# Performance work log

Hardware: AMD Instinct MI355X
Metric: run time of the kernel (lower is better)

## Reference

```python
import jax, jax.numpy as jnp
import numpy as np

jax.config.update("jax_enable_x64", True)  # original casts to double for covpool/SVD

BN_EPS = 1e-5


def setup_inputs() -> dict:
    key = jax.random.key(0)
    k1, k2 = jax.random.split(key)
    x = jax.random.normal(k1, (64, 2048, 14, 14), dtype=jnp.float32)
    conv_w = jax.random.normal(k2, (256, 2048), dtype=jnp.float32) * 0.02  # 1x1 conv kernel
    bn_gamma = jnp.ones((256,), dtype=jnp.float32)
    bn_beta = jnp.zeros((256,), dtype=jnp.float32)
    return {"x": x, "conv_w": conv_w, "bn_gamma": bn_gamma, "bn_beta": bn_beta}


def reference(x, conv_w, bn_gamma, bn_beta):
    # --- dimension reduction block: 1x1 conv (no bias) + BN (train mode) + ReLU ---
    y = jnp.einsum('oc,bchw->bohw', conv_w, x)  # [B,256,14,14]
    mean = y.mean(axis=(0, 2, 3), keepdims=True)
    var = y.var(axis=(0, 2, 3), keepdims=True)
    y = (y - mean) * jax.lax.rsqrt(var + BN_EPS)
    y = y * bn_gamma[None, :, None, None] + bn_beta[None, :, None, None]
    y = jnp.maximum(y, 0.0)

    # --- Covpool: x @ (I/M - 11^T/M^2) @ x^T, in float64 as original ---
    B, d, h, w = y.shape
    M = h * w
    z = y.reshape(B, d, M).astype(jnp.float64)
    zc = z - z.mean(axis=2, keepdims=True)          # centering == multiplying by I_hat
    cov = jnp.einsum('bim,bjm->bij', zc, zc) / M    # [B,d,d], symmetric PSD

    # --- Eigen decomposition (SVD of symmetric PSD == eigh), clamp tiny eigvals ---
    s, V = jnp.linalg.eigh(cov)                     # s: [B,d], V: [B,d,d]
    eps = jnp.finfo(jnp.float64).eps
    s = jnp.maximum(s, eps)

    # --- Power: matrix square root Q = V sqrt(S) V^T ---
    Q = jnp.einsum('bij,bj,bkj->bik', V, jnp.sqrt(s), V)  # [B,d,d]

    # --- upper-triangular (incl. diag) vectorization, row-major like torch triu ---
    iu = jnp.triu_indices(d)
    q_triv = Q[:, iu[0], iu[1]]                     # [B, d*(d+1)/2]
    return q_triv.astype(jnp.float32)
```

## Files before the change

kernel.cpp:

```cpp
#include <hip/hip_runtime.h>
#include <hip/hip_bf16.h>

static constexpr int B   = 64;
static constexpr int CIN = 2048;
static constexpr int O   = 256;
static constexpr int HW  = 196;
static constexpr int D   = 256;
static constexpr int TRI = 32896;
static constexpr int NQ_COUPLED = 5;
static constexpr size_t NELEM = (size_t)B * D * D;
static constexpr size_t YN    = (size_t)B * O * HW;

typedef unsigned short u16;
typedef unsigned short u16x4 __attribute__((ext_vector_type(4)));
typedef unsigned short u16x8 __attribute__((ext_vector_type(8)));
typedef __bf16         bf16x8 __attribute__((ext_vector_type(8)));
typedef float          f32x4 __attribute__((ext_vector_type(4)));

static __device__ __forceinline__ u16 f2bf(float x) {
    unsigned int u = __float_as_uint(x);
    u += 0x7FFFu + ((u >> 16) & 1u);
    return (u16)(u >> 16);
}
static __device__ __forceinline__ float bf2f(u16 h) {
    return __uint_as_float(((unsigned int)h) << 16);
}
static __device__ __forceinline__ f32x4 mm_bf16(u16x8 a, u16x8 b, f32x4 c) {
    return __builtin_amdgcn_mfma_f32_16x16x32_bf16(
        __builtin_bit_cast(bf16x8, a), __builtin_bit_cast(bf16x8, b), c, 0, 0, 0);
}

__global__ __launch_bounds__(256) void k_wsplit(const float* __restrict__ W,
                                                u16* __restrict__ Wh,
                                                u16* __restrict__ Wl) {
    const size_t i = (size_t)blockIdx.x * 256 + threadIdx.x;
    const float v = W[i];
    const u16 h = f2bf(v);
    Wh[i] = h;
    Wl[i] = f2bf(v - bf2f(h));
}

__global__ __launch_bounds__(256, 3) void k_conv(const float* __restrict__ x,
                                                 const u16* __restrict__ Wh,
                                                 const u16* __restrict__ Wl,
                                                 float* __restrict__ psum) {
    const int l   = blockIdx.x;
    const int xcd = l & 7, u = l >> 3;
    const int q   = xcd * 98 + u;
    const int ks  = q & 3;
    const int t2  = q >> 2;
    const int ot  = t2 & 1, gt = t2 >> 1;
    const int o0  = ot * 128;
    const int cbase = ks * 512;
    float* yp = psum + (size_t)ks * YN;

    const int tid = threadIdx.x;

    __shared__ u16 sW[2][128][40], sX[2][128][40];

    const int colX  = tid & 127;
    const int chalf = (tid >> 7) * 16;
    const int gX = gt * 128 + colX;
    const int bX = gX / 196;
    const int mX = gX - bX * 196;
    const size_t xbase = (size_t)bX * (CIN * HW) + mX;

    const int rW = tid >> 1, kq = (tid & 1) * 16;
    const u16* gWh = Wh + (size_t)(o0 + rW) * CIN + cbase + kq;
    const u16* gWl = Wl + (size_t)(o0 + rW) * CIN + cbase + kq;

    const int lane = tid & 63, w = tid >> 6;
    const int wr = w >> 1, wc = w & 1;
    const int lr = lane & 15, lg = lane >> 4, ko = lg << 3;

    f32x4 acc[4][4] = {};

    u16x8 pWh[2], pWl[2];
    float pX[16];
    u16x4 cXh[4], cXl[4];

    auto loadW = [&](int kb) {
        #pragma unroll
        for (int qq = 0; qq < 2; ++qq) {
            pWh[qq] = *(const u16x8*)&gWh[kb + qq * 8];
            pWl[qq] = *(const u16x8*)&gWl[kb + qq * 8];
        }
    };
    auto loadX = [&](int kb) {
        #pragma unroll
        for (int i = 0; i < 16; ++i)
            pX[i] = x[xbase + (size_t)(cbase + kb + chalf + i) * HW];
    };
    auto convX = [&]() {
        #pragma unroll
        for (int i = 0; i < 16; i += 4) {
            u16x4 vh, vl;
            #pragma unroll
            for (int j = 0; j < 4; ++j) {
                const float v = pX[i + j];
                const u16 h = f2bf(v);
                vh[j] = h;
                vl[j] = f2bf(v - bf2f(h));
            }
            cXh[i >> 2] = vh;
            cXl[i >> 2] = vl;
        }
    };
    auto storeWX = [&]() {
        #pragma unroll
        for (int qq = 0; qq < 2; ++qq) {
            *(u16x8*)&sW[0][rW][kq + qq * 8] = pWh[qq];
            *(u16x8*)&sW[1][rW][kq + qq * 8] = pWl[qq];
        }
        #pragma unroll
        for (int qq = 0; qq < 4; ++qq) {
            *(u16x4*)&sX[0][colX][chalf + qq * 4] = cXh[qq];
            *(u16x4*)&sX[1][colX][chalf + qq * 4] = cXl[qq];
        }
    };
    auto compute = [&]() {
        u16x8 fah[4], fal[4], fbh[4], fbl[4];
        #pragma unroll
        for (int f = 0; f < 4; ++f) {
            fah[f] = *(const u16x8*)&sW[0][wr * 64 + f * 16 + lr][ko];
            fal[f] = *(const u16x8*)&sW[1][wr * 64 + f * 16 + lr][ko];
            fbh[f] = *(const u16x8*)&sX[0][wc * 64 + f * 16 + lr][ko];
            fbl[f] = *(const u16x8*)&sX[1][wc * 64 + f * 16 + lr][ko];
        }
        #pragma unroll
        for (int fi = 0; fi < 4; ++fi)
            #pragma unroll
            for (int fj = 0; fj < 4; ++fj) {
                acc[fi][fj] = mm_bf16(fah[fi], fbh[fj], acc[fi][fj]);
                acc[fi][fj] = mm_bf16(fah[fi], fbl[fj], acc[fi][fj]);
                acc[fi][fj] = mm_bf16(fal[fi], fbh[fj], acc[fi][fj]);
            }
    };

    loadW(0); loadX(0); convX();
    for (int st = 0; st < 16; ++st) {
        __syncthreads();
        storeWX();
        __syncthreads();
        if (st < 15) { loadW((st + 1) * 32); loadX((st + 1) * 32); }
        compute();
        if (st < 15) convX();
    }

    #pragma unroll
    for (int fj = 0; fj < 4; ++fj) {
        const int gcol = gt * 128 + wc * 64 + fj * 16 + lr;
        const int bb = gcol / 196;
        const int mm = gcol - bb * 196;
        const size_t ybase = (size_t)bb * (O * HW) + mm;
        #pragma unroll
        for (int fi = 0; fi < 4; ++fi)
            #pragma unroll
            for (int r = 0; r < 4; ++r) {
                const int orow = o0 + wr * 64 + fi * 16 + (lg << 2) + r;
                yp[ybase + (size_t)orow * HW] = acc[fi][fj][r];
            }
    }
}

__global__ __launch_bounds__(256) void k_redy(const float* __restrict__ ps,
                                              float* __restrict__ y) {
    const size_t i = ((size_t)blockIdx.x * 256 + threadIdx.x) * 4;
    if (i >= YN) return;
    float4 a = *(const float4*)&ps[i];
    const float4 b = *(const float4*)&ps[YN + i];
    const float4 c = *(const float4*)&ps[2 * YN + i];
    const float4 d = *(const float4*)&ps[3 * YN + i];
    a.x += b.x + c.x + d.x; a.y += b.y + c.y + d.y;
    a.z += b.z + c.z + d.z; a.w += b.w + c.w + d.w;
    *(float4*)&y[i] = a;
}

__global__ __launch_bounds__(256) void k_bnstats(const float* __restrict__ y,
                                                 const float* __restrict__ gamma,
                                                 const float* __restrict__ beta,
                                                 float* __restrict__ scl,
                                                 float* __restrict__ shf) {
    const int o = blockIdx.x;
    const int tid = threadIdx.x;
    float s = 0.f, s2 = 0.f;
    if (tid < HW) {
        for (int b = 0; b < B; ++b) {
            const float v = y[((size_t)b * O + o) * HW + tid];
            s += v; s2 += v * v;
        }
    }
    #pragma unroll
    for (int msk = 32; msk; msk >>= 1) {
        s  += __shfl_xor(s,  msk);
        s2 += __shfl_xor(s2, msk);
    }
    __shared__ float rs[4], rs2[4];
    if ((tid & 63) == 0) { rs[tid >> 6] = s; rs2[tid >> 6] = s2; }
    __syncthreads();
    if (tid == 0) {
        const float N = (float)(B * HW);
        const float ts  = rs[0] + rs[1] + rs[2] + rs[3];
        const float ts2 = rs2[0] + rs2[1] + rs2[2] + rs2[3];
        const float mean = ts / N;
        const float var  = ts2 / N - mean * mean;
        const float sc = gamma[o] * rsqrtf(var + 1e-5f);
        scl[o] = sc;
        shf[o] = beta[o] - mean * sc;
    }
}

__global__ __launch_bounds__(64) void k_center(float* __restrict__ z,
                                               const float* __restrict__ scl,
                                               const float* __restrict__ shf) {
    const int row = blockIdx.x;
    const int o = row & 255;
    const int lane = threadIdx.x;
    const float sc = scl[o], sh = shf[o];
    float* zr = &z[(size_t)row * HW];
    float vals[4];
    float s = 0.f;
    #pragma unroll
    for (int q = 0; q < 4; ++q) {
        const int m = q * 64 + lane;
        float v = 0.f;
        if (m < HW) v = fmaxf(fmaf(zr[m], sc, sh), 0.f);
        vals[q] = v; s += v;
    }
    #pragma unroll
    for (int msk = 32; msk; msk >>= 1) s += __shfl_xor(s, msk);
    const float mean = s / (float)HW;
    #pragma unroll
    for (int q = 0; q < 4; ++q) {
        const int m = q * 64 + lane;
        if (m < HW) zr[m] = vals[q] - mean;
    }
}

__global__ __launch_bounds__(256) void k_cov(const float* __restrict__ z,
                                             float* __restrict__ covf) {
    const int b = blockIdx.y;
    const int jt = blockIdx.x & 3, it = blockIdx.x >> 2;
    const int i0 = it * 64, j0 = jt * 64;
    const int tid = threadIdx.x;
    const int tn = tid & 15, tmq = tid >> 4;

    __shared__ float sA[28][68], sB[28][68];
    double acc[4][4] = {};
    const float* zb = &z[(size_t)b * D * HW];

    for (int k0 = 0; k0 < HW; k0 += 28) {
        #pragma unroll
        for (int q = 0; q < 7; ++q) {
            const int idx = tid + q * 256;
            const int r = idx / 28, kk = idx % 28;
            sA[kk][r] = zb[(size_t)(i0 + r) * HW + k0 + kk];
            sB[kk][r] = zb[(size_t)(j0 + r) * HW + k0 + kk];
        }
        __syncthreads();
        #pragma unroll
        for (int kk = 0; kk < 28; ++kk) {
            const float4 av = *reinterpret_cast<const float4*>(&sA[kk][tmq << 2]);
            const float4 bv = *reinterpret_cast<const float4*>(&sB[kk][tn << 2]);
            const double aa[4] = {av.x, av.y, av.z, av.w};
            const double bb[4] = {bv.x, bv.y, bv.z, bv.w};
            #pragma unroll
            for (int i = 0; i < 4; ++i)
                #pragma unroll
                for (int j = 0; j < 4; ++j)
                    acc[i][j] = fma(aa[i], bb[j], acc[i][j]);
        }
        __syncthreads();
    }
    const double inv = 1.0 / (double)HW;
    #pragma unroll
    for (int i = 0; i < 4; ++i)
        #pragma unroll
        for (int j = 0; j < 4; ++j)
            covf[(size_t)b * D * D + (size_t)(i0 + (tmq << 2) + i) * D
                 + j0 + (tn << 2) + j] = (float)(acc[i][j] * inv);
}

__global__ __launch_bounds__(256) void k_lmax(const float* __restrict__ covf,
                                              double* __restrict__ cn) {
    const int b = blockIdx.x;
    const int tid = threadIdx.x;
    const float* A = &covf[(size_t)b * 65536];
    __shared__ float vs[256];
    __shared__ float red[4];
    vs[tid] = 1.f;
    __syncthreads();
    float lam = 1.f;
    for (int it = 0; it < 6; ++it) {
        float u0 = 0.f, u1 = 0.f, u2 = 0.f, u3 = 0.f;
        #pragma unroll 8
        for (int k = 0; k < D; k += 4) {
            u0 = fmaf(A[(size_t)(k + 0) * D + tid], vs[k + 0], u0);
            u1 = fmaf(A[(size_t)(k + 1) * D + tid], vs[k + 1], u1);
            u2 = fmaf(A[(size_t)(k + 2) * D + tid], vs[k + 2], u2);
            u3 = fmaf(A[(size_t)(k + 3) * D + tid], vs[k + 3], u3);
        }
        const float uu = (u0 + u1) + (u2 + u3);
        float sq = uu * uu;
        #pragma unroll
        for (int msk = 32; msk; msk >>= 1) sq += __shfl_xor(sq, msk);
        __syncthreads();
        if ((tid & 63) == 0) red[tid >> 6] = sq;
        __syncthreads();
        const float nrm = sqrtf(red[0] + red[1] + red[2] + red[3]) + 1e-30f;
        lam = nrm;
        vs[tid] = uu / nrm;
        __syncthreads();
    }
    if (tid == 0) cn[b] = (lam > 1e-30f) ? 1.25 * (double)lam : 1.0;
}

__global__ __launch_bounds__(256) void k_init(const float* __restrict__ covf,
                                              const double* __restrict__ cn,
                                              u16* __restrict__ Yh,
                                              u16* __restrict__ Yl) {
    const size_t e = (size_t)blockIdx.x * 256 + threadIdx.x;
    const int b = (int)(e >> 16);
    const int ij = (int)(e & 65535);
    const float diag = ((ij >> 8) == (ij & 255)) ? 1e-7f : 0.f;
    const float f = covf[e] / (float)cn[b] + diag;
    const u16 h = f2bf(f);
    Yh[e] = h;
    Yl[e] = f2bf(f - bf2f(h));
}

template <int MODE, int FUSED>
__global__ __launch_bounds__(256, 2) void k_mgemm(
        const u16* __restrict__ A0h, const u16* __restrict__ A0l,
        const u16* __restrict__ B0h, const u16* __restrict__ B0l,
        u16* __restrict__ C0h, u16* __restrict__ C0l,
        const u16* __restrict__ A1h, const u16* __restrict__ A1l,
        const u16* __restrict__ B1h, const u16* __restrict__ B1l,
        u16* __restrict__ C1h, u16* __restrict__ C1l,
        const double* __restrict__ cn, float* __restrict__ outp) {
    const int orig = blockIdx.x;
    const int xcd  = orig & 7;
    const int s    = orig >> 3;
    int batch, task, opz;
    if (FUSED) {
        const int bl  = s / 12;
        const int rem = s - bl * 12;
        opz  = rem >= 6;
        task = rem - opz * 6;
        batch = xcd * 8 + bl;
    } else {
        opz = 0;
        const int bl = s / 6;
        task = s - bl * 6;
        batch = xcd * 8 + bl;
    }

    const u16 *Ah, *Al, *Bh, *Bl;
    u16 *Ch, *Cl;
    if (opz == 0) { Ah = A0h; Al = A0l; Bh = B0h; Bl = B0l; Ch = C0h; Cl = C0l; }
    else          { Ah = A1h; Al = A1l; Bh = B1h; Bl = B1l; Ch = C1h; Cl = C1l; }

    const int it = task >> 2;
    const int jt = (task < 4) ? task : task - 2;
    const int i0 = it * 128, j0 = jt * 64;
    const size_t boff = (size_t)batch * 65536;
    Ah += boff; Al += boff; Bh += boff; Bl += boff; Ch += boff; Cl += boff;

    const int tid = threadIdx.x;
    __shared__ u16 sA[2][128][72];
    __shared__ u16 sB[2][64][72];

    const int rA = tid >> 1, khA = (tid & 1) * 32;
    const u16* gAh = Ah + (size_t)(i0 + rA) * 256 + khA;
    const u16* gAl = Al + (size_t)(i0 + rA) * 256 + khA;
    const int rB = tid >> 2, khB = (tid & 3) * 16;
    const u16* gBh = Bh + (size_t)(j0 + rB) * 256 + khB;
    const u16* gBl = Bl + (size_t)(j0 + rB) * 256 + khB;

    const int lane = tid & 63, w = tid >> 6;
    const int wr = w >> 1, wc = w & 1;
    const int lr = lane & 15, lg = lane >> 4, ko = lg << 3;

    f32x4 acc[4][2] = {};

    u16x8 pAh[4], pAl[4], pBh[2], pBl[2];
    auto g_load = [&](int kb) {
        #pragma unroll
        for (int qq = 0; qq < 4; ++qq) {
            pAh[qq] = *(const u16x8*)&gAh[kb + qq * 8];
            pAl[qq] = *(const u16x8*)&gAl[kb + qq * 8];
        }
        #pragma unroll
        for (int qq = 0; qq < 2; ++qq) {
            pBh[qq] = *(const u16x8*)&gBh[kb + qq * 8];
            pBl[qq] = *(const u16x8*)&gBl[kb + qq * 8];
        }
    };
    auto s_store = [&]() {
        #pragma unroll
        for (int qq = 0; qq < 4; ++qq) {
            *(u16x8*)&sA[0][rA][khA + qq * 8] = pAh[qq];
            *(u16x8*)&sA[1][rA][khA + qq * 8] = pAl[qq];
        }
        #pragma unroll
        for (int qq = 0; qq < 2; ++qq) {
            *(u16x8*)&sB[0][rB][khB + qq * 8] = pBh[qq];
            *(u16x8*)&sB[1][rB][khB + qq * 8] = pBl[qq];
        }
    };
    auto compute = [&]() {
        #pragma unroll
        for (int kr = 0; kr < 2; ++kr) {
            const int kk = kr * 32 + ko;
            u16x8 fah[4], fal[4], fbh[2], fbl[2];
            #pragma unroll
            for (int f = 0; f < 4; ++f) {
                fah[f] = *(const u16x8*)&sA[0][wr * 64 + f * 16 + lr][kk];
                fal[f] = *(const u16x8*)&sA[1][wr * 64 + f * 16 + lr][kk];
            }
            #pragma unroll
            for (int f = 0; f < 2; ++f) {
                fbh[f] = *(const u16x8*)&sB[0][wc * 32 + f * 16 + lr][kk];
                fbl[f] = *(const u16x8*)&sB[1][wc * 32 + f * 16 + lr][kk];
            }
            #pragma unroll
            for (int fi = 0; fi < 4; ++fi)
                #pragma unroll
                for (int fj = 0; fj < 2; ++fj) {
                    acc[fi][fj] = mm_bf16(fah[fi], fbh[fj], acc[fi][fj]);
                    acc[fi][fj] = mm_bf16(fah[fi], fbl[fj], acc[fi][fj]);
                    acc[fi][fj] = mm_bf16(fal[fi], fbh[fj], acc[fi][fj]);
                }
        }
    };

    g_load(0);
    for (int st = 0; st < 4; ++st) {
        __syncthreads();
        s_store();
        __syncthreads();
        if (st < 3) g_load((st + 1) * 64);
        compute();
    }

    const int orow = wr * 64 + (lg << 2);
    const int ocol = wc * 32 + lr;

    if (MODE == 3) {
        const double sc = sqrt(cn[batch]);
        #pragma unroll
        for (int fi = 0; fi < 4; ++fi)
            #pragma unroll
            for (int r = 0; r < 4; ++r) {
                const int gi = i0 + orow + fi * 16 + r;
                const size_t rowoff = (size_t)gi * D - ((size_t)gi * (gi - 1)) / 2;
                #pragma unroll
                for (int fj = 0; fj < 2; ++fj) {
                    const int gj = j0 + ocol + fj * 16;
                    if (gj >= gi)
                        outp[(size_t)batch * TRI + rowoff + (gj - gi)] =
                            (float)(sc * (double)acc[fi][fj][r]);
                }
            }
        return;
    }

    u16 hv[4][4][2], lv[4][4][2];
    #pragma unroll
    for (int fi = 0; fi < 4; ++fi)
        #pragma unroll
        for (int r = 0; r < 4; ++r) {
            const int gi = i0 + orow + fi * 16 + r;
            #pragma unroll
            for (int fj = 0; fj < 2; ++fj) {
                const int gj = j0 + ocol + fj * 16;
                float v = acc[fi][fj][r];
                if (MODE == 1) {
                    const size_t xo = (size_t)gi * 256 + gj;
                    const float xv = bf2f(Ah[xo]) + bf2f(Al[xo]);
                    v = (((gi == gj) ? 15.0f : 0.0f) - 10.0f * xv + 3.0f * v) * 0.125f;
                }
                const u16 h = f2bf(v);
                const u16 lo = f2bf(v - bf2f(h));
                const size_t co = (size_t)gi * 256 + gj;
                Ch[co] = h;
                Cl[co] = lo;
                hv[fi][r][fj] = h;
                lv[fi][r][fj] = lo;
            }
        }

    if (task == 2 || task == 3) {
        __syncthreads();
        u16 (*tH)[136] = reinterpret_cast<u16(*)[136]>(&sA[0][0][0]);
        u16 (*tL)[136] = reinterpret_cast<u16(*)[136]>(&sB[0][0][0]);
        #pragma unroll
        for (int fi = 0; fi < 4; ++fi)
            #pragma unroll
            for (int r = 0; r < 4; ++r) {
                const int li = orow + fi * 16 + r;
                #pragma unroll
                for (int fj = 0; fj < 2; ++fj) {
                    const int lj = ocol + fj * 16;
                    tH[lj][li] = hv[fi][r][fj];
                    tL[lj][li] = lv[fi][r][fj];
                }
            }
        __syncthreads();
        const int r2 = tid >> 2, c2 = (tid & 3) << 5;
        const size_t mo = (size_t)(j0 + r2) * 256 + i0 + c2;
        #pragma unroll
        for (int qq = 0; qq < 4; ++qq) {
            *(u16x8*)&Ch[mo + qq * 8] = *(const u16x8*)&tH[r2][c2 + qq * 8];
            *(u16x8*)&Cl[mo + qq * 8] = *(const u16x8*)&tL[r2][c2 + qq * 8];
        }
    }
}

extern "C" void kernel_launch(void* const* d_in, const int* in_sizes, int n_in,
                              void* d_out, int out_size, void* d_ws, size_t ws_size,
                              hipStream_t stream) {
    const float* x     = (const float*)d_in[0];
    const float* W     = (const float*)d_in[1];
    const float* gamma = (const float*)d_in[2];
    const float* beta  = (const float*)d_in[3];
    float* out = (float*)d_out;

    char* ws = (char*)d_ws;
    size_t off = 0;
    auto alloc = [&](size_t bytes) -> void* {
        void* p = ws + off;
        off += (bytes + 255) & ~(size_t)255;
        return p;
    };
    float*  y    = (float*)alloc(YN * sizeof(float));
    float*  covf = (float*)alloc(NELEM * sizeof(float));
    float*  scl  = (float*)alloc(O * sizeof(float));
    float*  shf  = (float*)alloc(O * sizeof(float));
    double* cn   = (double*)alloc(B * sizeof(double));
    u16*    Wh   = (u16*)alloc((size_t)O * CIN * sizeof(u16));
    u16*    Wl   = (u16*)alloc((size_t)O * CIN * sizeof(u16));
    u16* pl = (u16*)alloc(12 * NELEM * sizeof(u16));
    if (off > ws_size) return;
    u16 *YAh = pl,             *YAl = pl + NELEM;
    u16 *YBh = pl + 2 * NELEM, *YBl = pl + 3 * NELEM;
    u16 *MAh = pl + 4 * NELEM, *MAl = pl + 5 * NELEM;
    u16 *MBh = pl + 6 * NELEM, *MBl = pl + 7 * NELEM;
    u16 *Rh  = pl + 8 * NELEM, *Rl  = pl + 9 * NELEM;
    u16 *Uh  = pl + 10 * NELEM,*Ul  = pl + 11 * NELEM;
    float* psum = (float*)pl;

    k_wsplit <<<(O * CIN) / 256, 256, 0, stream>>>(W, Wh, Wl);
    k_conv   <<<784, 256, 0, stream>>>(x, Wh, Wl, psum);
    k_redy   <<<3136, 256, 0, stream>>>(psum, y);
    k_bnstats<<<O, 256, 0, stream>>>(y, gamma, beta, scl, shf);
    k_center <<<B * O, 64, 0, stream>>>(y, scl, shf);
    k_cov    <<<dim3(16, B), 256, 0, stream>>>(y, covf);
    k_lmax   <<<B, 256, 0, stream>>>(covf, cn);
    k_init   <<<B * 256, 256, 0, stream>>>(covf, cn, YAh, YAl);

    k_mgemm<1, 0><<<384, 256, 0, stream>>>(YAh, YAl, YAh, YAl, Rh, Rl,
                                           YAh, YAl, YAh, YAl, Rh, Rl, cn, out);
    k_mgemm<2, 0><<<384, 256, 0, stream>>>(YAh, YAl, Rh, Rl, YBh, YBl,
                                           YAh, YAl, Rh, Rl, YBh, YBl, cn, out);
    k_mgemm<2, 0><<<384, 256, 0, stream>>>(Rh, Rl, YBh, YBl, MBh, MBl,
                                           Rh, Rl, YBh, YBl, MBh, MBl, cn, out);

    u16 *Ych = YBh, *Ycl = YBl, *Yah = YAh, *Yal = YAl;
    u16 *Mch = MBh, *Mcl = MBl, *Mah = MAh, *Mal = MAl;
    for (int itq = 0; itq < NQ_COUPLED; ++itq) {
        k_mgemm<1, 0><<<384, 256, 0, stream>>>(Mch, Mcl, Mch, Mcl, Rh, Rl,
                                               Mch, Mcl, Mch, Mcl, Rh, Rl, cn, out);
        k_mgemm<2, 1><<<768, 256, 0, stream>>>(Ych, Ycl, Rh, Rl, Yah, Yal,
                                               Mch, Mcl, Rh, Rl, Uh, Ul, cn, out);
        k_mgemm<2, 0><<<384, 256, 0, stream>>>(Rh, Rl, Uh, Ul, Mah, Mal,
                                               Rh, Rl, Uh, Ul, Mah, Mal, cn, out);
        u16* t;
        t = Ych; Ych = Yah; Yah = t;  t = Ycl; Ycl = Yal; Yal = t;
        t = Mch; Mch = Mah; Mah = t;  t = Mcl; Mcl = Mal; Mal = t;
    }
    k_mgemm<1, 0><<<384, 256, 0, stream>>>(Mch, Mcl, Mch, Mcl, Rh, Rl,
                                           Mch, Mcl, Mch, Mcl, Rh, Rl, cn, out);
    k_mgemm<3, 0><<<384, 256, 0, stream>>>(Ych, Ycl, Rh, Rl, Uh, Ul,
                                           Ych, Ycl, Rh, Rl, Uh, Ul, cn, out);
}
```

Before: 508.3 us.

## Fuse split-K reduction into BN stats, vectorize init, prefetch MODE1 operand

The split-K partial-sum reduction kernel is removed and folded into the BN statistics kernel, which now sums the four partials with float4 loads, writes y, and accumulates the mean and variance sums in the same pass. The init kernel handles four elements per thread with vector loads and stores. The MODE 1 GEMM loads its X operand before the main loop instead of in the epilogue, so those loads can overlap the compute. The trade-offs are that BN stats now runs only 256 blocks over the full partial buffer, and the prefetched values add registers to the GEMM.

```diff
diff --git a/kernel.cpp b/kernel.cpp
--- a/kernel.cpp
+++ b/kernel.cpp
@@ -163,20 +163,8 @@
     }
 }
 
-__global__ __launch_bounds__(256) void k_redy(const float* __restrict__ ps,
-                                              float* __restrict__ y) {
-    const size_t i = ((size_t)blockIdx.x * 256 + threadIdx.x) * 4;
-    if (i >= YN) return;
-    float4 a = *(const float4*)&ps[i];
-    const float4 b = *(const float4*)&ps[YN + i];
-    const float4 c = *(const float4*)&ps[2 * YN + i];
-    const float4 d = *(const float4*)&ps[3 * YN + i];
-    a.x += b.x + c.x + d.x; a.y += b.y + c.y + d.y;
-    a.z += b.z + c.z + d.z; a.w += b.w + c.w + d.w;
-    *(float4*)&y[i] = a;
-}
-
-__global__ __launch_bounds__(256) void k_bnstats(const float* __restrict__ y,
+__global__ __launch_bounds__(256) void k_bnstats(const float* __restrict__ ps,
+                                                 float* __restrict__ y,
                                                  const float* __restrict__ gamma,
                                                  const float* __restrict__ beta,
                                                  float* __restrict__ scl,
@@ -184,11 +172,18 @@
     const int o = blockIdx.x;
     const int tid = threadIdx.x;
     float s = 0.f, s2 = 0.f;
-    if (tid < HW) {
-        for (int b = 0; b < B; ++b) {
-            const float v = y[((size_t)b * O + o) * HW + tid];
-            s += v; s2 += v * v;
-        }
+    for (int t = tid; t < 64 * 49; t += 256) {
+        const int b = t / 49, c = t - b * 49;
+        const size_t idx = ((size_t)b * O + o) * HW + c * 4;
+        float4 a = *(const float4*)&ps[idx];
+        const float4 p1 = *(const float4*)&ps[YN + idx];
+        const float4 p2 = *(const float4*)&ps[2 * YN + idx];
+        const float4 p3 = *(const float4*)&ps[3 * YN + idx];
+        a.x += p1.x + p2.x + p3.x; a.y += p1.y + p2.y + p3.y;
+        a.z += p1.z + p2.z + p3.z; a.w += p1.w + p2.w + p3.w;
+        *(float4*)&y[idx] = a;
+        s  += (a.x + a.y) + (a.z + a.w);
+        s2 += (a.x * a.x + a.y * a.y) + (a.z * a.z + a.w * a.w);
     }
     #pragma unroll
     for (int msk = 32; msk; msk >>= 1) {
@@ -319,14 +314,24 @@
                                               const double* __restrict__ cn,
                                               u16* __restrict__ Yh,
                                               u16* __restrict__ Yl) {
-    const size_t e = (size_t)blockIdx.x * 256 + threadIdx.x;
-    const int b = (int)(e >> 16);
-    const int ij = (int)(e & 65535);
-    const float diag = ((ij >> 8) == (ij & 255)) ? 1e-7f : 0.f;
-    const float f = covf[e] / (float)cn[b] + diag;
-    const u16 h = f2bf(f);
-    Yh[e] = h;
-    Yl[e] = f2bf(f - bf2f(h));
+    const size_t e4 = ((size_t)blockIdx.x * 256 + threadIdx.x) * 4;
+    const int b = (int)(e4 >> 16);
+    const int ij = (int)(e4 & 65535);
+    const int i = ij >> 8, j0_ = ij & 255;
+    const float4 cv = *(const float4*)&covf[e4];
+    const float inv = 1.f / (float)cn[b];
+    float f[4] = {cv.x * inv, cv.y * inv, cv.z * inv, cv.w * inv};
+    const int dk = i - j0_;
+    if (dk >= 0 && dk < 4) f[dk] += 1e-7f;
+    u16x4 h4, l4;
+    #pragma unroll
+    for (int k = 0; k < 4; ++k) {
+        const u16 h = f2bf(f[k]);
+        h4[k] = h;
+        l4[k] = f2bf(f[k] - bf2f(h));
+    }
+    *(u16x4*)&Yh[e4] = h4;
+    *(u16x4*)&Yl[e4] = l4;
 }
 
 template <int MODE, int FUSED>
@@ -380,6 +385,23 @@
     const int lane = tid & 63, w = tid >> 6;
     const int wr = w >> 1, wc = w & 1;
     const int lr = lane & 15, lg = lane >> 4, ko = lg << 3;
+    const int orow = wr * 64 + (lg << 2);
+    const int ocol = wc * 32 + lr;
+
+    float xv[4][4][2];
+    if (MODE == 1) {
+        #pragma unroll
+        for (int fi = 0; fi < 4; ++fi)
+            #pragma unroll
+            for (int r = 0; r < 4; ++r) {
+                const int gi = i0 + orow + fi * 16 + r;
+                #pragma unroll
+                for (int fj = 0; fj < 2; ++fj) {
+                    const size_t xo = (size_t)gi * 256 + j0 + ocol + fj * 16;
+                    xv[fi][r][fj] = bf2f(Ah[xo]) + bf2f(Al[xo]);
+                }
+            }
+    }
 
     f32x4 acc[4][2] = {};
 
@@ -442,9 +464,6 @@
         if (st < 3) g_load((st + 1) * 64);
         compute();
     }
-
-    const int orow = wr * 64 + (lg << 2);
-    const int ocol = wc * 32 + lr;
 
     if (MODE == 3) {
         const double sc = sqrt(cn[batch]);
@@ -476,9 +495,8 @@
                 const int gj = j0 + ocol + fj * 16;
                 float v = acc[fi][fj][r];
                 if (MODE == 1) {
-                    const size_t xo = (size_t)gi * 256 + gj;
-                    const float xv = bf2f(Ah[xo]) + bf2f(Al[xo]);
-                    v = (((gi == gj) ? 15.0f : 0.0f) - 10.0f * xv + 3.0f * v) * 0.125f;
+                    v = (((gi == gj) ? 15.0f : 0.0f)
+                         - 10.0f * xv[fi][r][fj] + 3.0f * v) * 0.125f;
                 }
                 const u16 h = f2bf(v);
                 const u16 lo = f2bf(v - bf2f(h));
@@ -552,12 +570,11 @@
 
     k_wsplit <<<(O * CIN) / 256, 256, 0, stream>>>(W, Wh, Wl);
     k_conv   <<<784, 256, 0, stream>>>(x, Wh, Wl, psum);
-    k_redy   <<<3136, 256, 0, stream>>>(psum, y);
-    k_bnstats<<<O, 256, 0, stream>>>(y, gamma, beta, scl, shf);
+    k_bnstats<<<O, 256, 0, stream>>>(psum, y, gamma, beta, scl, shf);
     k_center <<<B * O, 64, 0, stream>>>(y, scl, shf);
     k_cov    <<<dim3(16, B), 256, 0, stream>>>(y, covf);
     k_lmax   <<<B, 256, 0, stream>>>(covf, cn);
-    k_init   <<<B * 256, 256, 0, stream>>>(covf, cn, YAh, YAl);
+    k_init   <<<(int)(NELEM / 1024), 256, 0, stream>>>(covf, cn, YAh, YAl);
 
     k_mgemm<1, 0><<<384, 256, 0, stream>>>(YAh, YAl, YAh, YAl, Rh, Rl,
                                            YAh, YAl, YAh, YAl, Rh, Rl, cn, out);
```

Result: no change. 503.1 us (-1.0%).
